# Kernel optimization log

Hardware: AMD Instinct MI355X
Metric: run time of the kernel (lower is better)

The kernel has to match this reference:

```python
import jax, jax.numpy as jnp
import numpy as np

B, S, D, H, KV, HD = 2, 1024, 4096, 32, 8, 128
GROUP = H // KV


def setup_inputs() -> dict:
    key = jax.random.key(0)
    ks = jax.random.split(key, 9)
    x = jax.random.normal(ks[0], (B, S, D), dtype=jnp.float32)
    # RoPE tables: [max_seq_len, head_dim] (half-duplicated frequencies)
    pos = jnp.arange(S, dtype=jnp.float32)
    inv_freq = 1.0 / (10000.0 ** (jnp.arange(0, HD, 2, dtype=jnp.float32) / HD))
    freqs = pos[:, None] * inv_freq[None, :]            # [S, HD/2]
    emb = jnp.concatenate([freqs, freqs], axis=-1)      # [S, HD]
    cos, sin = jnp.cos(emb), jnp.sin(emb)
    # causal mask: True = masked
    mask = jnp.triu(jnp.ones((S, S), dtype=bool), 1)[None, None]  # [1,1,S,S]
    def qw(k, o, i):
        return jax.random.randint(k, (o, i), -127, 128, dtype=jnp.int8)
    wq = qw(ks[1], H * HD, D)
    wk = qw(ks[2], KV * HD, D)
    wv = qw(ks[3], KV * HD, D)
    wo = qw(ks[4], D, H * HD)
    sq = jnp.float32(0.02); sk = jnp.float32(0.02)
    sv = jnp.float32(0.02); so = jnp.float32(0.02)
    bq = jax.random.normal(ks[5], (H * HD,), jnp.float32) * 0.01
    bk = jax.random.normal(ks[6], (KV * HD,), jnp.float32) * 0.01
    bv = jax.random.normal(ks[7], (KV * HD,), jnp.float32) * 0.01
    return dict(x=x, mask=mask, cos=cos, sin=sin,
                wq=wq, bq=bq, sq=sq, wk=wk, bk=bk, sk=sk,
                wv=wv, bv=bv, sv=sv, wo=wo, so=so, start_pos=0)


def _deq_linear(x, w_int8, scale, bias):
    # dequantize-on-the-fly int8 linear: y = x @ (w.astype * scale).T + b
    w = w_int8.astype(x.dtype) * scale                  # [O, I]
    y = jnp.einsum('bsi,oi->bso', x, w)
    return y if bias is None else y + bias


def _rope(x, cos, sin, offset):
    # x: [b, s, h, hd]
    hd = x.shape[-1]
    x1, x2 = x[..., : hd // 2], x[..., hd // 2 :]
    s_len = x.shape[1]
    c = cos[offset : offset + s_len][None, :, None, :]
    s = sin[offset : offset + s_len][None, :, None, :]
    rotated = jnp.concatenate([-x2, x1], axis=-1)
    return (x * c + rotated * s).astype(x.dtype)


def reference(x, mask, cos, sin, wq, bq, sq, wk, bk, sk, wv, bv, sv, wo, so, start_pos):
    b, seq, _ = x.shape
    xq = _deq_linear(x, wq, sq, bq).reshape(b, seq, H, HD)
    xk = _deq_linear(x, wk, sk, bk).reshape(b, seq, KV, HD)
    xv = _deq_linear(x, wv, sv, bv).reshape(b, seq, KV, HD)
    xq = _rope(xq, cos, sin, start_pos)
    xk = _rope(xk, cos, sin, start_pos)
    # KV cache: start_pos=0 prefill -> cache[:start_pos+seq] == (xk, xv)
    kv_idx = jnp.arange(H) // GROUP                      # q head -> kv head
    keys = xk[:, :, kv_idx, :]                           # [b, kv_len, H, hd]
    values = xv[:, :, kv_idx, :]
    scores = jnp.einsum('bqhd,bkhd->bhqk', xq, keys) / np.sqrt(HD).astype(np.float32)
    scores = jnp.where(mask, -jnp.inf, scores)
    probs = jax.nn.softmax(scores, axis=-1)
    out = jnp.einsum('bhqk,bkhd->bqhd', probs, values).reshape(b, seq, H * HD)
    return _deq_linear(out, wo, so, None)
```

## Files before the change

### kernel.cpp

```cpp
#include <hip/hip_runtime.h>
#include <hip/hip_bf16.h>
#include <hip/hip_fp16.h>
#include <cstdint>

typedef _Float16 f16;
typedef _Float16 f16x8 __attribute__((ext_vector_type(8)));
typedef _Float16 f16x4 __attribute__((ext_vector_type(4)));
typedef float f32x4 __attribute__((ext_vector_type(4)));

#define DEV_INLINE __device__ __forceinline__

DEV_INLINE void async_ld16(const void* g, void* l) {
  __builtin_amdgcn_global_load_lds((const __attribute__((address_space(1))) void*)g,
                                   (__attribute__((address_space(3))) void*)l, 16, 0, 0);
}

template <int N>
DEV_INLINE void wait_vm() {
  static_assert(N >= 0 && N <= 12, "gate range");
  if constexpr (N == 0)  asm volatile("s_waitcnt vmcnt(0)" ::: "memory");
  if constexpr (N == 1)  asm volatile("s_waitcnt vmcnt(1)" ::: "memory");
  if constexpr (N == 2)  asm volatile("s_waitcnt vmcnt(2)" ::: "memory");
  if constexpr (N == 3)  asm volatile("s_waitcnt vmcnt(3)" ::: "memory");
  if constexpr (N == 4)  asm volatile("s_waitcnt vmcnt(4)" ::: "memory");
  if constexpr (N == 5)  asm volatile("s_waitcnt vmcnt(5)" ::: "memory");
  if constexpr (N == 6)  asm volatile("s_waitcnt vmcnt(6)" ::: "memory");
  if constexpr (N == 7)  asm volatile("s_waitcnt vmcnt(7)" ::: "memory");
  if constexpr (N == 8)  asm volatile("s_waitcnt vmcnt(8)" ::: "memory");
  if constexpr (N == 9)  asm volatile("s_waitcnt vmcnt(9)" ::: "memory");
  if constexpr (N == 10) asm volatile("s_waitcnt vmcnt(10)" ::: "memory");
  if constexpr (N == 11) asm volatile("s_waitcnt vmcnt(11)" ::: "memory");
  if constexpr (N == 12) asm volatile("s_waitcnt vmcnt(12)" ::: "memory");
}
DEV_INLINE void lgk0() {
  asm volatile("s_waitcnt lgkmcnt(0)" ::: "memory");
  __builtin_amdgcn_sched_barrier(0);
}


__global__ __launch_bounds__(256) void k_cast_x_split(const float* __restrict__ x,
                                                      f16* __restrict__ acat) {
  int idx = blockIdx.x * 256 + threadIdx.x;
  int i = idx * 4;
  if (i >= 2048 * 4096) return;
  float4 v = *(const float4*)&x[i];
  int row = i >> 12, col = i & 4095;
  f16 h0 = (f16)v.x, h1 = (f16)v.y, h2 = (f16)v.z, h3 = (f16)v.w;
  f16x4 hi = {h0, h1, h2, h3};
  f16x4 lo = {(f16)(v.x - (float)h0), (f16)(v.y - (float)h1),
              (f16)(v.z - (float)h2), (f16)(v.w - (float)h3)};
  size_t base = (size_t)row * 8192 + col;
  *(f16x4*)&acat[base] = hi;
  *(f16x4*)&acat[base + 4096] = lo;
}

__global__ __launch_bounds__(256) void k_cast_i32_f16(const int* __restrict__ w,
                                                      f16* __restrict__ out, int n) {
  int i = (blockIdx.x * 256 + threadIdx.x) * 4;
  if (i >= n) return;
  int4 v = *(const int4*)&w[i];
  f16x4 o = {(f16)(float)v.x, (f16)(float)v.y, (f16)(float)v.z, (f16)(float)v.w};
  *(f16x4*)&out[i] = o;
}

__global__ __launch_bounds__(256) void k_prep_bs(const float* bq, const float* bk, const float* bv,
                                                 const float* sq, const float* sk, const float* sv,
                                                 float* bias_cat, float* scale_cat) {
  int i = blockIdx.x * 256 + threadIdx.x;
  if (i >= 6144) return;
  float b, s;
  if (i < 4096)      { b = bq[i];        s = sq[0]; }
  else if (i < 5120) { b = bk[i - 4096]; s = sk[0]; }
  else               { b = bv[i - 5120]; s = sv[0]; }
  bias_cat[i] = b;
  scale_cat[i] = s;
}

template <int BM, int BN, int MODE>
__global__ __launch_bounds__(512) void k_gemm6(
    const f16* __restrict__ A, const f16* __restrict__ W,
    f16* __restrict__ o_hi, f16* __restrict__ o_lo, float* __restrict__ o_f32,
    const float* __restrict__ scale_vec, const float* __restrict__ bias_vec,
    const float* __restrict__ scale_scalar,
    int N, int K, int kmask, int ldw, int nym) {
  constexpr int WM = 2, WN = 4;
  constexpr int MR = BM / WM / 16;
  constexpr int NR = BN / WN / 16;
  constexpr int NH = NR / 2;
  constexpr int AKC = BM * 64;
  constexpr int BKC = BN * 64;
  constexpr int SLOT = 2 * (AKC + BKC);
  constexpr int LAH = AKC / 8192;
  constexpr int LBH = BKC / 8192;
  constexpr int GS = 2 * LBH + 3;
  constexpr int GT1 = 2 * LBH + 2;
  constexpr int GT2 = LBH + 1;
  extern __shared__ __align__(16) char lds[];

  const int t = threadIdx.x, w = t >> 6, ln = t & 63;
  const int lr = ln & 15, lg = ln >> 4;
  const int wn = w & 3, wm = w >> 2;

  const int nwg = gridDim.x;
  const int q8 = nwg >> 3, r8 = nwg & 7;
  const int xcd = blockIdx.x & 7, bidx = blockIdx.x >> 3;
  const int sid = (xcd < r8 ? xcd * (q8 + 1) : r8 * (q8 + 1) + (xcd - r8) * q8) + bidx;
  const int m0 = (sid % nym) * BM;
  const int n0 = (sid / nym) * BN;

  const f16* aSrc[LAH];
  const f16* bSrc[LBH];
#pragma unroll
  for (int l = 0; l < LAH; l++) {
    int ci = l * 512 + t, row = ci >> 2, c = ci & 3;
    aSrc[l] = A + (size_t)(m0 + row) * K + (c ^ ((row >> 1) & 3)) * 8;
  }
#pragma unroll
  for (int l = 0; l < LBH; l++) {
    int ci = l * 512 + t, row = ci >> 2, c = ci & 3;
    bSrc[l] = W + (size_t)(n0 + row) * ldw + (c ^ ((row >> 1) & 3)) * 8;
  }

  f32x4 acc[MR][NR] = {};
  f16x8 af[MR], bflo[NH], bfhi[NH];

  auto stageA = [&](int tt, int kc) {
    char* dst = lds + (tt & 1) * SLOT + kc * AKC;
    const int ko = tt * 64 + kc * 32;
#pragma unroll
    for (int l = 0; l < LAH; l++)
      async_ld16(aSrc[l] + ko, dst + (l * 512 + w * 64) * 16);
  };
  auto stageB = [&](int tt, int kc) {
    char* dst = lds + (tt & 1) * SLOT + 2 * AKC + kc * BKC;
    const int ko = ((tt * 64) & kmask) + kc * 32;
#pragma unroll
    for (int l = 0; l < LBH; l++)
      async_ld16(bSrc[l] + ko, dst + (l * 512 + w * 64) * 16);
  };
  auto readA = [&](int tt, int kc) {
    const char* base = lds + (tt & 1) * SLOT + kc * AKC;
#pragma unroll
    for (int mf = 0; mf < MR; mf++) {
      const int row = wm * (BM / WM) + mf * 16 + lr;
      af[mf] = *(const f16x8*)(base + row * 64 + (lg ^ ((row >> 1) & 3)) * 16);
    }
  };
  auto readB = [&](f16x8 (&dst)[NH], int tt, int nq, int kc) {
    const char* base = lds + (tt & 1) * SLOT + 2 * AKC + kc * BKC;
#pragma unroll
    for (int nf = 0; nf < NH; nf++) {
      const int row = wn * (BN / WN) + (nq * NH + nf) * 16 + lr;
      dst[nf] = *(const f16x8*)(base + row * 64 + (lg ^ ((row >> 1) & 3)) * 16);
    }
  };
  auto mma = [&](f16x8 (&b)[NH], int nq) {
    __builtin_amdgcn_s_setprio(1);
#pragma unroll
    for (int m = 0; m < MR; m++)
#pragma unroll
      for (int n = 0; n < NH; n++)
        acc[m][nq * NH + n] =
            __builtin_amdgcn_mfma_f32_16x16x32_f16(af[m], b[n], acc[m][nq * NH + n], 0, 0, 0);
    __builtin_amdgcn_s_setprio(0);
  };
  auto bar = [&]() { __builtin_amdgcn_s_barrier(); };

  const int NT = K >> 6;
  stageA(0, 0); stageB(0, 0); stageA(0, 1); stageB(0, 1);
  stageA(1, 0); stageB(1, 0); stageA(1, 1);
  wait_vm<GS>();
  bar();

  for (int tt = 0; tt + 2 < NT; ++tt) {
    stageB(tt + 1, 1);
    readA(tt, 0); readB(bflo, tt, 0, 0);
    bar(); lgk0(); mma(bflo, 0); bar();
    stageA(tt + 2, 0);
    readB(bfhi, tt, 1, 0);
    wait_vm<GS>();
    bar(); lgk0(); mma(bfhi, 1); bar();
    stageB(tt + 2, 0);
    readA(tt, 1); readB(bflo, tt, 0, 1);
    bar(); lgk0(); mma(bflo, 0); bar();
    stageA(tt + 2, 1);
    readB(bfhi, tt, 1, 1);
    wait_vm<GS>();
    bar(); lgk0(); mma(bfhi, 1); bar();
  }
  {
    const int tt = NT - 2;
    stageB(tt + 1, 1);
    readA(tt, 0); readB(bflo, tt, 0, 0);
    bar(); lgk0(); mma(bflo, 0); bar();
    readB(bfhi, tt, 1, 0);
    wait_vm<GT1>();
    bar(); lgk0(); mma(bfhi, 1); bar();
    readA(tt, 1); readB(bflo, tt, 0, 1);
    bar(); lgk0(); mma(bflo, 0); bar();
    readB(bfhi, tt, 1, 1);
    wait_vm<GT2>();
    bar(); lgk0(); mma(bfhi, 1); bar();
  }
  {
    const int tt = NT - 1;
    readA(tt, 0); readB(bflo, tt, 0, 0);
    bar(); lgk0(); mma(bflo, 0); bar();
    readB(bfhi, tt, 1, 0);
    wait_vm<0>();
    bar(); lgk0(); mma(bfhi, 1); bar();
    readA(tt, 1); readB(bflo, tt, 0, 1);
    bar(); lgk0(); mma(bflo, 0); bar();
    readB(bfhi, tt, 1, 1);
    bar(); lgk0(); mma(bfhi, 1);
  }

#pragma unroll
  for (int n = 0; n < NR; n++) {
    const int col = n0 + wn * (BN / WN) + n * 16 + lr;
    const float sc = (MODE == 0) ? scale_vec[col] : scale_scalar[0];
    const float bs = (MODE == 0) ? bias_vec[col] : 0.f;
#pragma unroll
    for (int m = 0; m < MR; m++)
#pragma unroll
      for (int r2 = 0; r2 < 4; r2++) {
        const int row = m0 + wm * (BM / WM) + m * 16 + lg * 4 + r2;
        const float v = acc[m][n][r2] * sc + bs;
        if constexpr (MODE == 0) {
          f16 h = (f16)v;
          o_hi[(size_t)row * N + col] = h;
          o_lo[(size_t)row * N + col] = (f16)(v - (float)h);
        } else {
          o_f32[(size_t)row * N + col] = v;
        }
      }
  }
}

__global__ __launch_bounds__(256) void k_rope(f16* __restrict__ XH, f16* __restrict__ XL,
                                              const float* __restrict__ cosT,
                                              const float* __restrict__ sinT,
                                              const int* __restrict__ sp) {
  int idx = blockIdx.x * 256 + threadIdx.x;
  if (idx >= 2048 * 40 * 64) return;
  int p = idx & 63;
  int hh = (idx >> 6) % 40;
  int tkn = idx / (40 * 64);
  int col = (hh < 32) ? hh * 128 + p : 4096 + (hh - 32) * 128 + p;
  size_t i1 = (size_t)tkn * 6144 + col, i2 = i1 + 64;
  float x1 = (float)XH[i1] + (float)XL[i1];
  float x2 = (float)XH[i2] + (float)XL[i2];
  int pos = (tkn & 1023) + sp[0];
  float c = cosT[pos * 128 + p], s = sinT[pos * 128 + p];
  float o1 = x1 * c - x2 * s;
  float o2 = x2 * c + x1 * s;
  f16 h1 = (f16)o1, h2 = (f16)o2;
  XH[i1] = h1; XL[i1] = (f16)(o1 - (float)h1);
  XH[i2] = h2; XL[i2] = (f16)(o2 - (float)h2);
}

__global__ __launch_bounds__(256) void k_attn(const f16* __restrict__ XH,
                                              const f16* __restrict__ XL,
                                              f16* __restrict__ out) {
  __shared__ __align__(16) f16 KsH[32 * 152];
  __shared__ __align__(16) f16 KsL[32 * 152];
  __shared__ __align__(16) f16 VT[128 * 40];
  __shared__ __align__(16) f16 Pb[4 * 16 * 40];
  const int t = threadIdx.x, w = t >> 6, l = t & 63;
  const int lr = l & 15, lg = l >> 4;
  const int qb = blockIdx.x, h = blockIdx.y, b = blockIdx.z;
  const int q0 = qb * 64, kvh = h >> 2;
  const size_t rs_ = 6144;
  const f16* Qh = XH + ((size_t)(b * 1024 + q0)) * rs_ + h * 128;
  const f16* Ql_ = XL + ((size_t)(b * 1024 + q0)) * rs_ + h * 128;
  const f16* KhG = XH + ((size_t)(b * 1024)) * rs_ + 4096 + kvh * 128;
  const f16* KlG = XL + ((size_t)(b * 1024)) * rs_ + 4096 + kvh * 128;
  const f16* VG = XH + ((size_t)(b * 1024)) * rs_ + 5120 + kvh * 128;

  f16x8 qh[4], ql[4];
  {
    size_t qoff = (size_t)(w * 16 + lr) * rs_ + lg * 8;
#pragma unroll
    for (int c = 0; c < 4; c++) {
      qh[c] = *(const f16x8*)(Qh + qoff + c * 32);
      ql[c] = *(const f16x8*)(Ql_ + qoff + c * 32);
    }
  }
  f32x4 accd[8] = {};
  float m_r[4], l_r[4];
#pragma unroll
  for (int r = 0; r < 4; r++) { m_r[r] = -1e30f; l_r[r] = 0.f; }

  const int nkv = q0 + 64;
  for (int kv0 = 0; kv0 < nkv; kv0 += 32) {
    __syncthreads();
#pragma unroll
    for (int i = 0; i < 2; i++) {
      int slot = i * 256 + t, row = slot >> 4, ch = slot & 15;
      size_t go = (size_t)(kv0 + row) * rs_ + ch * 8;
      *(f16x8*)&KsH[row * 152 + ch * 8] = *(const f16x8*)(KhG + go);
      *(f16x8*)&KsL[row * 152 + ch * 8] = *(const f16x8*)(KlG + go);
    }
#pragma unroll
    for (int i = 0; i < 2; i++) {
      int slot = i * 256 + t, row = slot & 31, d8 = slot >> 5;
      f16x8 vv = *(const f16x8*)(VG + (size_t)(kv0 + row) * rs_ + d8 * 8);
#pragma unroll
      for (int j = 0; j < 8; j++) VT[(d8 * 8 + j) * 40 + row] = vv[j];
    }
    __syncthreads();

    f32x4 sc[2] = {};
#pragma unroll
    for (int cb = 0; cb < 2; cb++)
#pragma unroll
      for (int c = 0; c < 4; c++) {
        const f16x8 kh = *(const f16x8*)&KsH[(cb * 16 + lr) * 152 + c * 32 + lg * 8];
        const f16x8 kl = *(const f16x8*)&KsL[(cb * 16 + lr) * 152 + c * 32 + lg * 8];
        sc[cb] = __builtin_amdgcn_mfma_f32_16x16x32_f16(qh[c], kh, sc[cb], 0, 0, 0);
        sc[cb] = __builtin_amdgcn_mfma_f32_16x16x32_f16(qh[c], kl, sc[cb], 0, 0, 0);
        sc[cb] = __builtin_amdgcn_mfma_f32_16x16x32_f16(ql[c], kh, sc[cb], 0, 0, 0);
      }

    const float scale = 0.088388347648318447f;
    float alpha[4], pv[2][4];
#pragma unroll
    for (int r = 0; r < 4; r++) {
      const int qg = q0 + w * 16 + lg * 4 + r;
      float mx = -1e30f;
#pragma unroll
      for (int cb = 0; cb < 2; cb++) {
        const int kg = kv0 + cb * 16 + lr;
        float s = sc[cb][r] * scale;
        s = (kg <= qg) ? s : -1e30f;
        pv[cb][r] = s;
        mx = fmaxf(mx, s);
      }
      mx = fmaxf(mx, __shfl_xor(mx, 1));
      mx = fmaxf(mx, __shfl_xor(mx, 2));
      mx = fmaxf(mx, __shfl_xor(mx, 4));
      mx = fmaxf(mx, __shfl_xor(mx, 8));
      const float mn = fmaxf(m_r[r], mx);
      alpha[r] = __expf(m_r[r] - mn);
      m_r[r] = mn;
      float rsum = 0.f;
#pragma unroll
      for (int cb = 0; cb < 2; cb++) {
        const int kg = kv0 + cb * 16 + lr;
        const float p = (kg <= qg) ? __expf(pv[cb][r] - mn) : 0.f;
        pv[cb][r] = p;
        rsum += p;
      }
      rsum += __shfl_xor(rsum, 1);
      rsum += __shfl_xor(rsum, 2);
      rsum += __shfl_xor(rsum, 4);
      rsum += __shfl_xor(rsum, 8);
      l_r[r] = l_r[r] * alpha[r] + rsum;
    }

    f16* Pw = &Pb[w * 16 * 40];
#pragma unroll
    for (int r = 0; r < 4; r++)
#pragma unroll
      for (int cb = 0; cb < 2; cb++)
        Pw[(lg * 4 + r) * 40 + cb * 16 + lr] = (f16)pv[cb][r];
    const f16x8 pf = *(const f16x8*)&Pw[lr * 40 + lg * 8];

#pragma unroll
    for (int dc = 0; dc < 8; dc++) {
      const f16x8 vf = *(const f16x8*)&VT[(dc * 16 + lr) * 40 + lg * 8];
#pragma unroll
      for (int r = 0; r < 4; r++) accd[dc][r] *= alpha[r];
      accd[dc] = __builtin_amdgcn_mfma_f32_16x16x32_f16(pf, vf, accd[dc], 0, 0, 0);
    }
  }

#pragma unroll
  for (int dc = 0; dc < 8; dc++)
#pragma unroll
    for (int r = 0; r < 4; r++) {
      const int row = b * 1024 + q0 + w * 16 + lg * 4 + r;
      out[(size_t)row * 4096 + h * 128 + dc * 16 + lr] = (f16)(accd[dc][r] / l_r[r]);
    }
}

extern "C" void kernel_launch(void* const* d_in, const int* in_sizes, int n_in,
                              void* d_out, int out_size, void* d_ws, size_t ws_size,
                              hipStream_t stream) {
  const float* x = (const float*)d_in[0];
  const float* cosT = (const float*)d_in[2];
  const float* sinT = (const float*)d_in[3];
  const int* wq = (const int*)d_in[4];
  const float* bq = (const float*)d_in[5];
  const float* sq = (const float*)d_in[6];
  const int* wk = (const int*)d_in[7];
  const float* bk = (const float*)d_in[8];
  const float* sk = (const float*)d_in[9];
  const int* wv = (const int*)d_in[10];
  const float* bv = (const float*)d_in[11];
  const float* sv = (const float*)d_in[12];
  const int* wo = (const int*)d_in[13];
  const float* so = (const float*)d_in[14];
  const int* sp = (const int*)d_in[15];

  char* ws = (char*)d_ws;
  f16* Acat = (f16*)ws;
  f16* Wcat = (f16*)(ws + 33554432);
  f16* XH = (f16*)(ws + 83886080);
  f16* XL = (f16*)(ws + 109051904);
  f16* AO = (f16*)(ws + 134217728);
  float* biasv = (float*)(ws + 150994944);
  float* scalev = (float*)(ws + 151019520);

  hipFuncSetAttribute(reinterpret_cast<const void*>(&k_gemm6<128, 384, 0>),
                      hipFuncAttributeMaxDynamicSharedMemorySize, 131072);
  hipFuncSetAttribute(reinterpret_cast<const void*>(&k_gemm6<128, 256, 1>),
                      hipFuncAttributeMaxDynamicSharedMemorySize, 98304);

  k_cast_x_split<<<8192, 256, 0, stream>>>(x, Acat);
  k_cast_i32_f16<<<16384, 256, 0, stream>>>(wq, Wcat, 16777216);
  k_cast_i32_f16<<<4096, 256, 0, stream>>>(wk, Wcat + (size_t)4096 * 4096, 4194304);
  k_cast_i32_f16<<<4096, 256, 0, stream>>>(wv, Wcat + (size_t)5120 * 4096, 4194304);
  k_prep_bs<<<24, 256, 0, stream>>>(bq, bk, bv, sq, sk, sv, biasv, scalev);

  k_gemm6<128, 384, 0><<<256, 512, 131072, stream>>>(
      Acat, Wcat, XH, XL, nullptr, scalev, biasv, nullptr, 6144, 8192, 4095, 4096, 16);

  k_rope<<<20480, 256, 0, stream>>>(XH, XL, cosT, sinT, sp);

  f16* Wo_ = Acat;
  k_cast_i32_f16<<<16384, 256, 0, stream>>>(wo, Wo_, 16777216);

  k_attn<<<dim3(16, 32, 2), 256, 0, stream>>>(XH, XL, AO);

  k_gemm6<128, 256, 1><<<256, 512, 98304, stream>>>(
      AO, Wo_, nullptr, nullptr, (float*)d_out, nullptr, nullptr, so, 4096, 4096,
      0x7fffffff, 4096, 16);
}
```

Before: 496.9 us.

## Double-buffer attention K/V tiles with async LDS loads and merge weight-prep launches

Result: slower. 511.7 us (+3.0%).

```diff
diff --git a/kernel.cpp b/kernel.cpp
--- a/kernel.cpp
+++ b/kernel.cpp
@@ -63,17 +63,29 @@
   *(f16x4*)&out[i] = o;
 }
 
-__global__ __launch_bounds__(256) void k_prep_bs(const float* bq, const float* bk, const float* bv,
-                                                 const float* sq, const float* sk, const float* sv,
-                                                 float* bias_cat, float* scale_cat) {
+__global__ __launch_bounds__(256) void k_prep_w(
+    const int* __restrict__ wq, const int* __restrict__ wk, const int* __restrict__ wv,
+    const float* __restrict__ bq, const float* __restrict__ bk, const float* __restrict__ bv,
+    const float* __restrict__ sq, const float* __restrict__ sk, const float* __restrict__ sv,
+    f16* __restrict__ wcat, float* __restrict__ bias_cat, float* __restrict__ scale_cat) {
   int i = blockIdx.x * 256 + threadIdx.x;
-  if (i >= 6144) return;
-  float b, s;
-  if (i < 4096)      { b = bq[i];        s = sq[0]; }
-  else if (i < 5120) { b = bk[i - 4096]; s = sk[0]; }
-  else               { b = bv[i - 5120]; s = sv[0]; }
-  bias_cat[i] = b;
-  scale_cat[i] = s;
+  if (i < 6291456) {
+    int e = i * 4, row = e >> 12, col = e & 4095;
+    int4 v;
+    if (row < 4096)      v = *(const int4*)&wq[(size_t)row * 4096 + col];
+    else if (row < 5120) v = *(const int4*)&wk[(size_t)(row - 4096) * 4096 + col];
+    else                 v = *(const int4*)&wv[(size_t)(row - 5120) * 4096 + col];
+    f16x4 o = {(f16)(float)v.x, (f16)(float)v.y, (f16)(float)v.z, (f16)(float)v.w};
+    *(f16x4*)&wcat[e] = o;
+  }
+  if (i < 6144) {
+    float b, s;
+    if (i < 4096)      { b = bq[i];        s = sq[0]; }
+    else if (i < 5120) { b = bk[i - 4096]; s = sk[0]; }
+    else               { b = bv[i - 5120]; s = sv[0]; }
+    bias_cat[i] = b;
+    scale_cat[i] = s;
+  }
 }
 
 template <int BM, int BN, int MODE>
@@ -259,12 +271,12 @@
   XH[i2] = h2; XL[i2] = (f16)(o2 - (float)h2);
 }
 
-__global__ __launch_bounds__(256) void k_attn(const f16* __restrict__ XH,
-                                              const f16* __restrict__ XL,
-                                              f16* __restrict__ out) {
-  __shared__ __align__(16) f16 KsH[32 * 152];
-  __shared__ __align__(16) f16 KsL[32 * 152];
-  __shared__ __align__(16) f16 VT[128 * 40];
+__global__ __launch_bounds__(256) void k_attn2(const f16* __restrict__ XH,
+                                               const f16* __restrict__ XL,
+                                               f16* __restrict__ out) {
+  __shared__ __align__(16) f16 KsH[2][32 * 128];
+  __shared__ __align__(16) f16 KsL[2][32 * 128];
+  __shared__ __align__(16) f16 VT[2][128 * 40];
   __shared__ __align__(16) f16 Pb[4 * 16 * 40];
   const int t = threadIdx.x, w = t >> 6, l = t & 63;
   const int lr = l & 15, lg = l >> 4;
@@ -291,36 +303,63 @@
 #pragma unroll
   for (int r = 0; r < 4; r++) { m_r[r] = -1e30f; l_r[r] = 0.f; }
 
-  const int nkv = q0 + 64;
-  for (int kv0 = 0; kv0 < nkv; kv0 += 32) {
-    __syncthreads();
+  f16x8 vreg[2];
+  auto stageK = [&](int kv0, int buf) {
 #pragma unroll
     for (int i = 0; i < 2; i++) {
-      int slot = i * 256 + t, row = slot >> 4, ch = slot & 15;
-      size_t go = (size_t)(kv0 + row) * rs_ + ch * 8;
-      *(f16x8*)&KsH[row * 152 + ch * 8] = *(const f16x8*)(KhG + go);
-      *(f16x8*)&KsL[row * 152 + ch * 8] = *(const f16x8*)(KlG + go);
-    }
+      int ci = i * 256 + t, row = ci >> 4, ch = ci & 15;
+      int chs = ch ^ (row & 7);
+      size_t go = (size_t)(kv0 + row) * rs_ + chs * 8;
+      char* dH = (char*)&KsH[buf][0] + (i * 256 + w * 64) * 16;
+      char* dL = (char*)&KsL[buf][0] + (i * 256 + w * 64) * 16;
+      async_ld16(KhG + go, dH);
+      async_ld16(KlG + go, dL);
+    }
+  };
+  auto loadV = [&](int kv0) {
 #pragma unroll
     for (int i = 0; i < 2; i++) {
       int slot = i * 256 + t, row = slot & 31, d8 = slot >> 5;
-      f16x8 vv = *(const f16x8*)(VG + (size_t)(kv0 + row) * rs_ + d8 * 8);
-#pragma unroll
-      for (int j = 0; j < 8; j++) VT[(d8 * 8 + j) * 40 + row] = vv[j];
-    }
-    __syncthreads();
+      vreg[i] = *(const f16x8*)(VG + (size_t)(kv0 + row) * rs_ + d8 * 8);
+    }
+  };
+  auto writeVT = [&](int buf) {
+#pragma unroll
+    for (int i = 0; i < 2; i++) {
+      int slot = i * 256 + t, row = slot & 31, d8 = slot >> 5;
+#pragma unroll
+      for (int j = 0; j < 8; j++) VT[buf][(d8 * 8 + j) * 40 + row] = vreg[i][j];
+    }
+  };
+
+  const int NT = (q0 + 64) >> 5;
+  stageK(0, 0); loadV(0);
+  wait_vm<0>();
+  __builtin_amdgcn_s_barrier();
+  writeVT(0);
+  asm volatile("s_waitcnt lgkmcnt(0)" ::: "memory");
+  __builtin_amdgcn_s_barrier();
+
+  for (int tt = 0; tt < NT; ++tt) {
+    const int cur = tt & 1;
+    const int kv0 = tt * 32;
+    const bool pf = (tt + 1 < NT);
+    if (pf) { stageK(kv0 + 32, cur ^ 1); loadV(kv0 + 32); }
 
     f32x4 sc[2] = {};
 #pragma unroll
-    for (int cb = 0; cb < 2; cb++)
+    for (int cb = 0; cb < 2; cb++) {
+      const int krow = cb * 16 + lr;
 #pragma unroll
       for (int c = 0; c < 4; c++) {
-        const f16x8 kh = *(const f16x8*)&KsH[(cb * 16 + lr) * 152 + c * 32 + lg * 8];
-        const f16x8 kl = *(const f16x8*)&KsL[(cb * 16 + lr) * 152 + c * 32 + lg * 8];
+        const int gidx = ((c * 4 + lg) ^ (krow & 7)) * 8;
+        const f16x8 kh = *(const f16x8*)&KsH[cur][krow * 128 + gidx];
+        const f16x8 kl = *(const f16x8*)&KsL[cur][krow * 128 + gidx];
         sc[cb] = __builtin_amdgcn_mfma_f32_16x16x32_f16(qh[c], kh, sc[cb], 0, 0, 0);
         sc[cb] = __builtin_amdgcn_mfma_f32_16x16x32_f16(qh[c], kl, sc[cb], 0, 0, 0);
         sc[cb] = __builtin_amdgcn_mfma_f32_16x16x32_f16(ql[c], kh, sc[cb], 0, 0, 0);
       }
+    }
 
     const float scale = 0.088388347648318447f;
     float alpha[4], pv[2][4];
@@ -364,14 +403,22 @@
 #pragma unroll
       for (int cb = 0; cb < 2; cb++)
         Pw[(lg * 4 + r) * 40 + cb * 16 + lr] = (f16)pv[cb][r];
-    const f16x8 pf = *(const f16x8*)&Pw[lr * 40 + lg * 8];
+    const f16x8 pf_ = *(const f16x8*)&Pw[lr * 40 + lg * 8];
 
 #pragma unroll
     for (int dc = 0; dc < 8; dc++) {
-      const f16x8 vf = *(const f16x8*)&VT[(dc * 16 + lr) * 40 + lg * 8];
+      const f16x8 vf = *(const f16x8*)&VT[cur][(dc * 16 + lr) * 40 + lg * 8];
 #pragma unroll
       for (int r = 0; r < 4; r++) accd[dc][r] *= alpha[r];
-      accd[dc] = __builtin_amdgcn_mfma_f32_16x16x32_f16(pf, vf, accd[dc], 0, 0, 0);
+      accd[dc] = __builtin_amdgcn_mfma_f32_16x16x32_f16(pf_, vf, accd[dc], 0, 0, 0);
+    }
+
+    if (pf) {
+      wait_vm<0>();
+      __builtin_amdgcn_s_barrier();
+      writeVT(cur ^ 1);
+      asm volatile("s_waitcnt lgkmcnt(0)" ::: "memory");
+      __builtin_amdgcn_s_barrier();
     }
   }
 
@@ -418,10 +465,8 @@
                       hipFuncAttributeMaxDynamicSharedMemorySize, 98304);
 
   k_cast_x_split<<<8192, 256, 0, stream>>>(x, Acat);
-  k_cast_i32_f16<<<16384, 256, 0, stream>>>(wq, Wcat, 16777216);
-  k_cast_i32_f16<<<4096, 256, 0, stream>>>(wk, Wcat + (size_t)4096 * 4096, 4194304);
-  k_cast_i32_f16<<<4096, 256, 0, stream>>>(wv, Wcat + (size_t)5120 * 4096, 4194304);
-  k_prep_bs<<<24, 256, 0, stream>>>(bq, bk, bv, sq, sk, sv, biasv, scalev);
+  k_prep_w<<<24576, 256, 0, stream>>>(wq, wk, wv, bq, bk, bv, sq, sk, sv,
+                                      Wcat, biasv, scalev);
 
   k_gemm6<128, 384, 0><<<256, 512, 131072, stream>>>(
       Acat, Wcat, XH, XL, nullptr, scalev, biasv, nullptr, 6144, 8192, 4095, 4096, 16);
@@ -431,7 +476,7 @@
   f16* Wo_ = Acat;
   k_cast_i32_f16<<<16384, 256, 0, stream>>>(wo, Wo_, 16777216);
 
-  k_attn<<<dim3(16, 32, 2), 256, 0, stream>>>(XH, XL, AO);
+  k_attn2<<<dim3(16, 32, 2), 256, 0, stream>>>(XH, XL, AO);
 
   k_gemm6<128, 256, 1><<<256, 512, 98304, stream>>>(
       AO, Wo_, nullptr, nullptr, (float*)d_out, nullptr, nullptr, so, 4096, 4096,
```

## Restructure GEMM into 4-slot K=32 pipeline and fuse weight-cast launches

Applied to the files above, without the earlier changes.

After: 495.4 us. About the same (-0.3%).

```diff
diff --git a/kernel.cpp b/kernel.cpp
--- a/kernel.cpp
+++ b/kernel.cpp
@@ -32,8 +32,18 @@
   if constexpr (N == 11) asm volatile("s_waitcnt vmcnt(11)" ::: "memory");
   if constexpr (N == 12) asm volatile("s_waitcnt vmcnt(12)" ::: "memory");
 }
-DEV_INLINE void lgk0() {
-  asm volatile("s_waitcnt lgkmcnt(0)" ::: "memory");
+
+template <int N>
+DEV_INLINE void wait_lgk() {
+  static_assert(N >= 0 && N <= 15, "lgk range");
+  if constexpr (N == 0) asm volatile("s_waitcnt lgkmcnt(0)" ::: "memory");
+  if constexpr (N == 1) asm volatile("s_waitcnt lgkmcnt(1)" ::: "memory");
+  if constexpr (N == 2) asm volatile("s_waitcnt lgkmcnt(2)" ::: "memory");
+  if constexpr (N == 3) asm volatile("s_waitcnt lgkmcnt(3)" ::: "memory");
+  if constexpr (N == 4) asm volatile("s_waitcnt lgkmcnt(4)" ::: "memory");
+  if constexpr (N == 5) asm volatile("s_waitcnt lgkmcnt(5)" ::: "memory");
+  if constexpr (N == 6) asm volatile("s_waitcnt lgkmcnt(6)" ::: "memory");
+  if constexpr (N == 7) asm volatile("s_waitcnt lgkmcnt(7)" ::: "memory");
   __builtin_amdgcn_sched_barrier(0);
 }
 
@@ -63,21 +73,33 @@
   *(f16x4*)&out[i] = o;
 }
 
-__global__ __launch_bounds__(256) void k_prep_bs(const float* bq, const float* bk, const float* bv,
-                                                 const float* sq, const float* sk, const float* sv,
-                                                 float* bias_cat, float* scale_cat) {
+__global__ __launch_bounds__(256) void k_prep_w(
+    const int* __restrict__ wq, const int* __restrict__ wk, const int* __restrict__ wv,
+    const float* __restrict__ bq, const float* __restrict__ bk, const float* __restrict__ bv,
+    const float* __restrict__ sq, const float* __restrict__ sk, const float* __restrict__ sv,
+    f16* __restrict__ wcat, float* __restrict__ bias_cat, float* __restrict__ scale_cat) {
   int i = blockIdx.x * 256 + threadIdx.x;
-  if (i >= 6144) return;
-  float b, s;
-  if (i < 4096)      { b = bq[i];        s = sq[0]; }
-  else if (i < 5120) { b = bk[i - 4096]; s = sk[0]; }
-  else               { b = bv[i - 5120]; s = sv[0]; }
-  bias_cat[i] = b;
-  scale_cat[i] = s;
+  if (i < 6291456) {
+    int e = i * 4, row = e >> 12, col = e & 4095;
+    int4 v;
+    if (row < 4096)      v = *(const int4*)&wq[(size_t)row * 4096 + col];
+    else if (row < 5120) v = *(const int4*)&wk[(size_t)(row - 4096) * 4096 + col];
+    else                 v = *(const int4*)&wv[(size_t)(row - 5120) * 4096 + col];
+    f16x4 o = {(f16)(float)v.x, (f16)(float)v.y, (f16)(float)v.z, (f16)(float)v.w};
+    *(f16x4*)&wcat[e] = o;
+  }
+  if (i < 6144) {
+    float b, s;
+    if (i < 4096)      { b = bq[i];        s = sq[0]; }
+    else if (i < 5120) { b = bk[i - 4096]; s = sk[0]; }
+    else               { b = bv[i - 5120]; s = sv[0]; }
+    bias_cat[i] = b;
+    scale_cat[i] = s;
+  }
 }
 
 template <int BM, int BN, int MODE>
-__global__ __launch_bounds__(512) void k_gemm6(
+__global__ __launch_bounds__(512) void k_gemm7(
     const f16* __restrict__ A, const f16* __restrict__ W,
     f16* __restrict__ o_hi, f16* __restrict__ o_lo, float* __restrict__ o_f32,
     const float* __restrict__ scale_vec, const float* __restrict__ bias_vec,
@@ -87,14 +109,13 @@
   constexpr int MR = BM / WM / 16;
   constexpr int NR = BN / WN / 16;
   constexpr int NH = NR / 2;
-  constexpr int AKC = BM * 64;
-  constexpr int BKC = BN * 64;
-  constexpr int SLOT = 2 * (AKC + BKC);
-  constexpr int LAH = AKC / 8192;
-  constexpr int LBH = BKC / 8192;
-  constexpr int GS = 2 * LBH + 3;
-  constexpr int GT1 = 2 * LBH + 2;
-  constexpr int GT2 = LBH + 1;
+  constexpr int ATB = BM * 64;
+  constexpr int BTB = BN * 64;
+  constexpr int SLOT = ATB + BTB;
+  constexpr int LA = ATB / 8192;
+  constexpr int LB = BTB / 8192;
+  constexpr int SOPS = LA + LB;
+  constexpr int GS = 2 * SOPS;
   extern __shared__ __align__(16) char lds[];
 
   const int t = threadIdx.x, w = t >> 6, ln = t & 63;
@@ -108,124 +129,148 @@
   const int m0 = (sid % nym) * BM;
   const int n0 = (sid / nym) * BN;
 
-  const f16* aSrc[LAH];
-  const f16* bSrc[LBH];
-#pragma unroll
-  for (int l = 0; l < LAH; l++) {
+  const f16* aSrc[LA];
+  const f16* bSrc[LB];
+#pragma unroll
+  for (int l = 0; l < LA; l++) {
     int ci = l * 512 + t, row = ci >> 2, c = ci & 3;
     aSrc[l] = A + (size_t)(m0 + row) * K + (c ^ ((row >> 1) & 3)) * 8;
   }
 #pragma unroll
-  for (int l = 0; l < LBH; l++) {
+  for (int l = 0; l < LB; l++) {
     int ci = l * 512 + t, row = ci >> 2, c = ci & 3;
     bSrc[l] = W + (size_t)(n0 + row) * ldw + (c ^ ((row >> 1) & 3)) * 8;
   }
 
   f32x4 acc[MR][NR] = {};
-  f16x8 af[MR], bflo[NH], bfhi[NH];
-
-  auto stageA = [&](int tt, int kc) {
-    char* dst = lds + (tt & 1) * SLOT + kc * AKC;
-    const int ko = tt * 64 + kc * 32;
-#pragma unroll
-    for (int l = 0; l < LAH; l++)
+  f16x8 af0[MR], af1[MR], blo0[NH], blo1[NH], bfhi[NH];
+
+  auto stage = [&](int tt, int slot) {
+    char* dst = lds + slot * SLOT;
+    const int ko = tt * 32;
+    const int kb = ko & kmask;
+#pragma unroll
+    for (int l = 0; l < LA; l++)
       async_ld16(aSrc[l] + ko, dst + (l * 512 + w * 64) * 16);
-  };
-  auto stageB = [&](int tt, int kc) {
-    char* dst = lds + (tt & 1) * SLOT + 2 * AKC + kc * BKC;
-    const int ko = ((tt * 64) & kmask) + kc * 32;
-#pragma unroll
-    for (int l = 0; l < LBH; l++)
-      async_ld16(bSrc[l] + ko, dst + (l * 512 + w * 64) * 16);
-  };
-  auto readA = [&](int tt, int kc) {
-    const char* base = lds + (tt & 1) * SLOT + kc * AKC;
+#pragma unroll
+    for (int l = 0; l < LB; l++)
+      async_ld16(bSrc[l] + kb, dst + ATB + (l * 512 + w * 64) * 16);
+  };
+  auto readANlo = [&](f16x8 (&af)[MR], f16x8 (&blo)[NH], int slot) {
+    const char* base = lds + slot * SLOT;
 #pragma unroll
     for (int mf = 0; mf < MR; mf++) {
       const int row = wm * (BM / WM) + mf * 16 + lr;
       af[mf] = *(const f16x8*)(base + row * 64 + (lg ^ ((row >> 1) & 3)) * 16);
     }
-  };
-  auto readB = [&](f16x8 (&dst)[NH], int tt, int nq, int kc) {
-    const char* base = lds + (tt & 1) * SLOT + 2 * AKC + kc * BKC;
+    const char* bb = base + ATB;
 #pragma unroll
     for (int nf = 0; nf < NH; nf++) {
-      const int row = wn * (BN / WN) + (nq * NH + nf) * 16 + lr;
-      dst[nf] = *(const f16x8*)(base + row * 64 + (lg ^ ((row >> 1) & 3)) * 16);
-    }
-  };
-  auto mma = [&](f16x8 (&b)[NH], int nq) {
+      const int row = wn * (BN / WN) + nf * 16 + lr;
+      blo[nf] = *(const f16x8*)(bb + row * 64 + (lg ^ ((row >> 1) & 3)) * 16);
+    }
+  };
+  auto readBhi = [&](int slot) {
+    const char* bb = lds + slot * SLOT + ATB;
+#pragma unroll
+    for (int nf = 0; nf < NH; nf++) {
+      const int row = wn * (BN / WN) + (NH + nf) * 16 + lr;
+      bfhi[nf] = *(const f16x8*)(bb + row * 64 + (lg ^ ((row >> 1) & 3)) * 16);
+    }
+  };
+  auto mma_lo = [&](f16x8 (&af)[MR], f16x8 (&blo)[NH]) {
     __builtin_amdgcn_s_setprio(1);
 #pragma unroll
     for (int m = 0; m < MR; m++)
 #pragma unroll
       for (int n = 0; n < NH; n++)
-        acc[m][nq * NH + n] =
-            __builtin_amdgcn_mfma_f32_16x16x32_f16(af[m], b[n], acc[m][nq * NH + n], 0, 0, 0);
+        acc[m][n] = __builtin_amdgcn_mfma_f32_16x16x32_f16(af[m], blo[n], acc[m][n], 0, 0, 0);
     __builtin_amdgcn_s_setprio(0);
   };
+  auto mma_hi = [&](f16x8 (&af)[MR]) {
+    __builtin_amdgcn_s_setprio(1);
+#pragma unroll
+    for (int m = 0; m < MR; m++)
+#pragma unroll
+      for (int n = 0; n < NH; n++)
+        acc[m][NH + n] =
+            __builtin_amdgcn_mfma_f32_16x16x32_f16(af[m], bfhi[n], acc[m][NH + n], 0, 0, 0);
+    __builtin_amdgcn_s_setprio(0);
+  };
   auto bar = [&]() { __builtin_amdgcn_s_barrier(); };
 
-  const int NT = K >> 6;
-  stageA(0, 0); stageB(0, 0); stageA(0, 1); stageB(0, 1);
-  stageA(1, 0); stageB(1, 0); stageA(1, 1);
+  const int NT = K >> 5;
+  int sc = 0, sn = 1, s3 = 3;
+  auto rot = [&]() { int tmp = sc; sc = sn; sn = (sn + 1) & 3; s3 = tmp; };
+
+  stage(0, 0); stage(1, 1); stage(2, 2);
   wait_vm<GS>();
   bar();
-
-  for (int tt = 0; tt + 2 < NT; ++tt) {
-    stageB(tt + 1, 1);
-    readA(tt, 0); readB(bflo, tt, 0, 0);
-    bar(); lgk0(); mma(bflo, 0); bar();
-    stageA(tt + 2, 0);
-    readB(bfhi, tt, 1, 0);
+  readANlo(af0, blo0, 0);
+
+  auto tile_full = [&](f16x8 (&afC)[MR], f16x8 (&bloC)[NH],
+                       f16x8 (&afN)[MR], f16x8 (&bloN)[NH], int tt) {
+    readBhi(sc);
+    wait_lgk<NH>();
+    mma_lo(afC, bloC);
+    bar();
+    stage(tt + 3, s3);
     wait_vm<GS>();
-    bar(); lgk0(); mma(bfhi, 1); bar();
-    stageB(tt + 2, 0);
-    readA(tt, 1); readB(bflo, tt, 0, 1);
-    bar(); lgk0(); mma(bflo, 0); bar();
-    stageA(tt + 2, 1);
-    readB(bfhi, tt, 1, 1);
-    wait_vm<GS>();
-    bar(); lgk0(); mma(bfhi, 1); bar();
-  }
+    bar();
+    readANlo(afN, bloN, sn);
+    wait_lgk<MR + NH>();
+    mma_hi(afC);
+    rot();
+  };
+
+  for (int tt = 0; tt + 5 < NT; tt += 2) {
+    tile_full(af0, blo0, af1, blo1, tt);
+    tile_full(af1, blo1, af0, blo0, tt + 1);
+  }
+  tile_full(af0, blo0, af1, blo1, NT - 4);
   {
-    const int tt = NT - 2;
-    stageB(tt + 1, 1);
-    readA(tt, 0); readB(bflo, tt, 0, 0);
-    bar(); lgk0(); mma(bflo, 0); bar();
-    readB(bfhi, tt, 1, 0);
-    wait_vm<GT1>();
-    bar(); lgk0(); mma(bfhi, 1); bar();
-    readA(tt, 1); readB(bflo, tt, 0, 1);
-    bar(); lgk0(); mma(bflo, 0); bar();
-    readB(bfhi, tt, 1, 1);
-    wait_vm<GT2>();
-    bar(); lgk0(); mma(bfhi, 1); bar();
+    readBhi(sc);
+    wait_lgk<NH>();
+    mma_lo(af1, blo1);
+    bar();
+    wait_vm<SOPS>();
+    bar();
+    readANlo(af0, blo0, sn);
+    wait_lgk<MR + NH>();
+    mma_hi(af1);
+    rot();
   }
   {
-    const int tt = NT - 1;
-    readA(tt, 0); readB(bflo, tt, 0, 0);
-    bar(); lgk0(); mma(bflo, 0); bar();
-    readB(bfhi, tt, 1, 0);
+    readBhi(sc);
+    wait_lgk<NH>();
+    mma_lo(af0, blo0);
+    bar();
     wait_vm<0>();
-    bar(); lgk0(); mma(bfhi, 1); bar();
-    readA(tt, 1); readB(bflo, tt, 0, 1);
-    bar(); lgk0(); mma(bflo, 0); bar();
-    readB(bfhi, tt, 1, 1);
-    bar(); lgk0(); mma(bfhi, 1);
+    bar();
+    readANlo(af1, blo1, sn);
+    wait_lgk<MR + NH>();
+    mma_hi(af0);
+    rot();
+  }
+  {
+    readBhi(sc);
+    wait_lgk<NH>();
+    mma_lo(af1, blo1);
+    wait_lgk<0>();
+    mma_hi(af1);
   }
 
 #pragma unroll
   for (int n = 0; n < NR; n++) {
     const int col = n0 + wn * (BN / WN) + n * 16 + lr;
-    const float sc = (MODE == 0) ? scale_vec[col] : scale_scalar[0];
+    const float sc2 = (MODE == 0) ? scale_vec[col] : scale_scalar[0];
     const float bs = (MODE == 0) ? bias_vec[col] : 0.f;
 #pragma unroll
     for (int m = 0; m < MR; m++)
 #pragma unroll
       for (int r2 = 0; r2 < 4; r2++) {
         const int row = m0 + wm * (BM / WM) + m * 16 + lg * 4 + r2;
-        const float v = acc[m][n][r2] * sc + bs;
+        const float v = acc[m][n][r2] * sc2 + bs;
         if constexpr (MODE == 0) {
           f16 h = (f16)v;
           o_hi[(size_t)row * N + col] = h;
@@ -412,18 +457,16 @@
   float* biasv = (float*)(ws + 150994944);
   float* scalev = (float*)(ws + 151019520);
 
-  hipFuncSetAttribute(reinterpret_cast<const void*>(&k_gemm6<128, 384, 0>),
+  hipFuncSetAttribute(reinterpret_cast<const void*>(&k_gemm7<128, 384, 0>),
                       hipFuncAttributeMaxDynamicSharedMemorySize, 131072);
-  hipFuncSetAttribute(reinterpret_cast<const void*>(&k_gemm6<128, 256, 1>),
+  hipFuncSetAttribute(reinterpret_cast<const void*>(&k_gemm7<128, 256, 1>),
                       hipFuncAttributeMaxDynamicSharedMemorySize, 98304);
 
   k_cast_x_split<<<8192, 256, 0, stream>>>(x, Acat);
-  k_cast_i32_f16<<<16384, 256, 0, stream>>>(wq, Wcat, 16777216);
-  k_cast_i32_f16<<<4096, 256, 0, stream>>>(wk, Wcat + (size_t)4096 * 4096, 4194304);
-  k_cast_i32_f16<<<4096, 256, 0, stream>>>(wv, Wcat + (size_t)5120 * 4096, 4194304);
-  k_prep_bs<<<24, 256, 0, stream>>>(bq, bk, bv, sq, sk, sv, biasv, scalev);
-
-  k_gemm6<128, 384, 0><<<256, 512, 131072, stream>>>(
+  k_prep_w<<<24576, 256, 0, stream>>>(wq, wk, wv, bq, bk, bv, sq, sk, sv,
+                                      Wcat, biasv, scalev);
+
+  k_gemm7<128, 384, 0><<<256, 512, 131072, stream>>>(
       Acat, Wcat, XH, XL, nullptr, scalev, biasv, nullptr, 6144, 8192, 4095, 4096, 16);
 
   k_rope<<<20480, 256, 0, stream>>>(XH, XL, cosT, sinT, sp);
@@ -433,7 +476,7 @@
 
   k_attn<<<dim3(16, 32, 2), 256, 0, stream>>>(XH, XL, AO);
 
-  k_gemm6<128, 256, 1><<<256, 512, 98304, stream>>>(
+  k_gemm7<128, 256, 1><<<256, 512, 98304, stream>>>(
       AO, Wo_, nullptr, nullptr, (float*)d_out, nullptr, nullptr, so, 4096, 4096,
       0x7fffffff, 4096, 16);
 }
```

## Widen attention blocks to 128 queries and fuse QKV weight cast kernels

Applied to the files above, without the earlier changes.

New measurement: 476.9 us. 1.04x faster.

```diff
diff --git a/kernel.cpp b/kernel.cpp
--- a/kernel.cpp
+++ b/kernel.cpp
@@ -63,17 +63,29 @@
   *(f16x4*)&out[i] = o;
 }
 
-__global__ __launch_bounds__(256) void k_prep_bs(const float* bq, const float* bk, const float* bv,
-                                                 const float* sq, const float* sk, const float* sv,
-                                                 float* bias_cat, float* scale_cat) {
+__global__ __launch_bounds__(256) void k_prep_w(
+    const int* __restrict__ wq, const int* __restrict__ wk, const int* __restrict__ wv,
+    const float* __restrict__ bq, const float* __restrict__ bk, const float* __restrict__ bv,
+    const float* __restrict__ sq, const float* __restrict__ sk, const float* __restrict__ sv,
+    f16* __restrict__ wcat, float* __restrict__ bias_cat, float* __restrict__ scale_cat) {
   int i = blockIdx.x * 256 + threadIdx.x;
-  if (i >= 6144) return;
-  float b, s;
-  if (i < 4096)      { b = bq[i];        s = sq[0]; }
-  else if (i < 5120) { b = bk[i - 4096]; s = sk[0]; }
-  else               { b = bv[i - 5120]; s = sv[0]; }
-  bias_cat[i] = b;
-  scale_cat[i] = s;
+  if (i < 6291456) {
+    int e = i * 4, row = e >> 12, col = e & 4095;
+    int4 v;
+    if (row < 4096)      v = *(const int4*)&wq[(size_t)row * 4096 + col];
+    else if (row < 5120) v = *(const int4*)&wk[(size_t)(row - 4096) * 4096 + col];
+    else                 v = *(const int4*)&wv[(size_t)(row - 5120) * 4096 + col];
+    f16x4 o = {(f16)(float)v.x, (f16)(float)v.y, (f16)(float)v.z, (f16)(float)v.w};
+    *(f16x4*)&wcat[e] = o;
+  }
+  if (i < 6144) {
+    float b, s;
+    if (i < 4096)      { b = bq[i];        s = sq[0]; }
+    else if (i < 5120) { b = bk[i - 4096]; s = sk[0]; }
+    else               { b = bv[i - 5120]; s = sv[0]; }
+    bias_cat[i] = b;
+    scale_cat[i] = s;
+  }
 }
 
 template <int BM, int BN, int MODE>
@@ -259,17 +271,23 @@
   XH[i2] = h2; XL[i2] = (f16)(o2 - (float)h2);
 }
 
-__global__ __launch_bounds__(256) void k_attn(const f16* __restrict__ XH,
-                                              const f16* __restrict__ XL,
-                                              f16* __restrict__ out) {
+__global__ __launch_bounds__(512) void k_attn3(const f16* __restrict__ XH,
+                                               const f16* __restrict__ XL,
+                                               f16* __restrict__ out) {
   __shared__ __align__(16) f16 KsH[32 * 152];
   __shared__ __align__(16) f16 KsL[32 * 152];
   __shared__ __align__(16) f16 VT[128 * 40];
-  __shared__ __align__(16) f16 Pb[4 * 16 * 40];
+  __shared__ __align__(16) f16 Pb[8 * 16 * 40];
   const int t = threadIdx.x, w = t >> 6, l = t & 63;
   const int lr = l & 15, lg = l >> 4;
-  const int qb = blockIdx.x, h = blockIdx.y, b = blockIdx.z;
-  const int q0 = qb * 64, kvh = h >> 2;
+  const int id = blockIdx.x;
+  const int kvh = id & 7;
+  const int j = id >> 3;
+  const int qb = j & 7;
+  const int hg = (j >> 3) & 3;
+  const int b = j >> 5;
+  const int h = kvh * 4 + hg;
+  const int q0 = qb * 128;
   const size_t rs_ = 6144;
   const f16* Qh = XH + ((size_t)(b * 1024 + q0)) * rs_ + h * 128;
   const f16* Ql_ = XL + ((size_t)(b * 1024 + q0)) * rs_ + h * 128;
@@ -291,22 +309,20 @@
 #pragma unroll
   for (int r = 0; r < 4; r++) { m_r[r] = -1e30f; l_r[r] = 0.f; }
 
-  const int nkv = q0 + 64;
+  const int nkv = q0 + 128;
   for (int kv0 = 0; kv0 < nkv; kv0 += 32) {
     __syncthreads();
-#pragma unroll
-    for (int i = 0; i < 2; i++) {
-      int slot = i * 256 + t, row = slot >> 4, ch = slot & 15;
+    {
+      int row = t >> 4, ch = t & 15;
       size_t go = (size_t)(kv0 + row) * rs_ + ch * 8;
       *(f16x8*)&KsH[row * 152 + ch * 8] = *(const f16x8*)(KhG + go);
       *(f16x8*)&KsL[row * 152 + ch * 8] = *(const f16x8*)(KlG + go);
     }
-#pragma unroll
-    for (int i = 0; i < 2; i++) {
-      int slot = i * 256 + t, row = slot & 31, d8 = slot >> 5;
+    {
+      int row = t & 31, d8 = t >> 5;
       f16x8 vv = *(const f16x8*)(VG + (size_t)(kv0 + row) * rs_ + d8 * 8);
 #pragma unroll
-      for (int j = 0; j < 8; j++) VT[(d8 * 8 + j) * 40 + row] = vv[j];
+      for (int jj = 0; jj < 8; jj++) VT[(d8 * 8 + jj) * 40 + row] = vv[jj];
     }
     __syncthreads();
 
@@ -418,10 +434,8 @@
                       hipFuncAttributeMaxDynamicSharedMemorySize, 98304);
 
   k_cast_x_split<<<8192, 256, 0, stream>>>(x, Acat);
-  k_cast_i32_f16<<<16384, 256, 0, stream>>>(wq, Wcat, 16777216);
-  k_cast_i32_f16<<<4096, 256, 0, stream>>>(wk, Wcat + (size_t)4096 * 4096, 4194304);
-  k_cast_i32_f16<<<4096, 256, 0, stream>>>(wv, Wcat + (size_t)5120 * 4096, 4194304);
-  k_prep_bs<<<24, 256, 0, stream>>>(bq, bk, bv, sq, sk, sv, biasv, scalev);
+  k_prep_w<<<24576, 256, 0, stream>>>(wq, wk, wv, bq, bk, bv, sq, sk, sv,
+                                      Wcat, biasv, scalev);
 
   k_gemm6<128, 384, 0><<<256, 512, 131072, stream>>>(
       Acat, Wcat, XH, XL, nullptr, scalev, biasv, nullptr, 6144, 8192, 4095, 4096, 16);
@@ -431,7 +445,7 @@
   f16* Wo_ = Acat;
   k_cast_i32_f16<<<16384, 256, 0, stream>>>(wo, Wo_, 16777216);
 
-  k_attn<<<dim3(16, 32, 2), 256, 0, stream>>>(XH, XL, AO);
+  k_attn3<<<512, 512, 0, stream>>>(XH, XL, AO);
 
   k_gemm6<128, 256, 1><<<256, 512, 98304, stream>>>(
       AO, Wo_, nullptr, nullptr, (float*)d_out, nullptr, nullptr, so, 4096, 4096,
```
